# Kernel optimization log

Hardware: AMD Instinct MI355X
Metric: run time of the kernel (lower is better)

## Reference

```python
import jax, jax.numpy as jnp
import numpy as np

# --- static config (matches init_kwargs / input_specs) ---
N_GRAPHS = 32
NODES = 1000          # num_nodes per graph
N = N_GRAPHS * NODES  # 32000 total nodes
F_IN = 128            # num_features
E_DIM = 16            # edge_attr_dim
H, C = 4, 16          # heads, GAT_dim
HC = H * C            # 64
E = 512000            # edges (before self-loops)
PROJ = 8              # proj_nodes
OUT = 256             # output_dim
NEG_SLOPE = 0.2       # PyG GATConv default


def setup_inputs() -> dict:
    key = jax.random.key(0)
    ks = jax.random.split(key, 20)
    s = 0.1
    return {
        "x": jax.random.normal(ks[0], (N, F_IN), jnp.float32),
        "edge_attr": jax.random.normal(ks[1], (E, E_DIM), jnp.float32),
        # layer 0 (input_conv): F_IN -> H*C
        "W0":   jax.random.normal(ks[2], (F_IN, HC), jnp.float32) * s,
        "a_s0": jax.random.normal(ks[3], (H, C), jnp.float32) * s,
        "a_d0": jax.random.normal(ks[4], (H, C), jnp.float32) * s,
        "W_e0": jax.random.normal(ks[5], (E_DIM, HC), jnp.float32) * s,
        "a_e0": jax.random.normal(ks[6], (H, C), jnp.float32) * s,
        "b0":   jnp.zeros((HC,), jnp.float32),
        # layers 1..2 stacked: HC -> H*C
        "Wg":   jax.random.normal(ks[7], (2, HC, HC), jnp.float32) * s,
        "a_sg": jax.random.normal(ks[8], (2, H, C), jnp.float32) * s,
        "a_dg": jax.random.normal(ks[9], (2, H, C), jnp.float32) * s,
        "W_eg": jax.random.normal(ks[10], (2, E_DIM, HC), jnp.float32) * s,
        "a_eg": jax.random.normal(ks[11], (2, H, C), jnp.float32) * s,
        "bg":   jnp.zeros((2, HC), jnp.float32),
        # node_proj: HC -> PROJ ; fc_out: NODES*PROJ -> OUT
        "Wp": jax.random.normal(ks[12], (HC, PROJ), jnp.float32) * s,
        "bp": jnp.zeros((PROJ,), jnp.float32),
        "Wo": jax.random.normal(ks[13], (NODES * PROJ, OUT), jnp.float32) * (s / 4),
        "bo": jnp.zeros((OUT,), jnp.float32),
        "edge_index": jax.random.randint(ks[14], (2, E), 0, N, jnp.int32),
        "batch": jnp.repeat(jnp.arange(N_GRAPHS, dtype=jnp.int32), NODES),
    }


def _gat_layer(x, src, dst, eattr, W, a_s, a_d, W_e, a_e, b):
    """PyG GATConv (concat=True, shared src/dst lin, edge_dim) forward."""
    xl = (x @ W).reshape(N, H, C)                       # [N,H,C]
    al_s = jnp.sum(xl * a_s, axis=-1)                   # [N,H]
    al_d = jnp.sum(xl * a_d, axis=-1)                   # [N,H]
    el = (eattr @ W_e).reshape(-1, H, C)                # [Ef,H,C]
    al_e = jnp.sum(el * a_e, axis=-1)                   # [Ef,H]
    logits = jax.nn.leaky_relu(al_s[src] + al_d[dst] + al_e, NEG_SLOPE)
    # segment softmax over destination nodes (every node has a self-loop)
    mx = jax.ops.segment_max(logits, dst, num_segments=N)
    p = jnp.exp(logits - mx[dst])
    denom = jax.ops.segment_sum(p, dst, num_segments=N)
    alpha = p / denom[dst]                               # [Ef,H]
    out = jax.ops.segment_sum(xl[src] * alpha[..., None], dst, num_segments=N)
    return out.reshape(N, HC) + b


def reference(x, edge_attr, W0, a_s0, a_d0, W_e0, a_e0, b0,
              Wg, a_sg, a_dg, W_eg, a_eg, bg,
              Wp, bp, Wo, bo, edge_index, batch):
    src, dst = edge_index[0], edge_index[1]
    # PyG add_self_loops with fill_value='mean': per-dst mean of incoming edge_attr
    deg = jax.ops.segment_sum(jnp.ones((E,), edge_attr.dtype), dst, num_segments=N)
    loop_attr = jax.ops.segment_sum(edge_attr, dst, num_segments=N) / jnp.maximum(deg, 1.0)[:, None]
    loops = jnp.arange(N, dtype=src.dtype)
    src_f = jnp.concatenate([src, loops])
    dst_f = jnp.concatenate([dst, loops])
    ea_f = jnp.concatenate([edge_attr, loop_attr], axis=0)   # [E+N, E_DIM]

    h = jax.nn.relu(_gat_layer(x, src_f, dst_f, ea_f, W0, a_s0, a_d0, W_e0, a_e0, b0))
    for i in range(2):
        h = jax.nn.relu(_gat_layer(h, src_f, dst_f, ea_f,
                                   Wg[i], a_sg[i], a_dg[i], W_eg[i], a_eg[i], bg[i]))
    h = jax.nn.relu(h @ Wp + bp)                             # [N, PROJ]
    B = batch.shape[0] // NODES                              # static batch count
    h = h.reshape(B, NODES * PROJ)
    return h @ Wo + bo                                       # [B, OUT]
```

## Files before the change

kernel.cpp:

```cpp
#include <hip/hip_runtime.h>
#include <hip/hip_bf16.h>
#include <hip/hip_fp16.h>

#define N_NODES 32000
#define FIN     128
#define E_EDGES 512000
#define EF_EDGES 544000
#define HC      64
#define NGRAPH  32
#define PROJ    8
#define OUT_DIM 256

static __device__ inline unsigned short f2bf(float f) {
  unsigned int x = __float_as_uint(f);
  unsigned int r = (x + 0x7fffu + ((x >> 16) & 1u)) >> 16;
  return (unsigned short)r;
}
static __device__ inline float bf2f(unsigned short u) {
  return __uint_as_float((unsigned int)u << 16);
}
static __device__ inline unsigned short f2h(float f) {
  return __half_as_ushort(__float2half(f));
}
static __device__ inline float h2f(unsigned short u) {
  return __half2float(__ushort_as_half(u));
}

__global__ __launch_bounds__(256) void zero_kernel(int* __restrict__ deg) {
  deg[blockIdx.x * 256 + threadIdx.x] = 0;
}

__global__ __launch_bounds__(256) void deg_kernel(const int* __restrict__ ei,
                                                  int* __restrict__ deg) {
  int e = blockIdx.x * 256 + threadIdx.x;
  atomicAdd(&deg[ei[E_EDGES + e]], 1);
}

__global__ __launch_bounds__(256) void scan1_kernel(const int* __restrict__ deg,
                                                    int* __restrict__ offs,
                                                    int* __restrict__ bsum) {
  int idx = blockIdx.x * 256 + threadIdx.x;
  int lane = threadIdx.x & 63;
  int w = threadIdx.x >> 6;
  int v = deg[idx] + 1;
  int s = v;
#pragma unroll
  for (int off = 1; off < 64; off <<= 1) {
    int t = __shfl_up(s, off);
    if (lane >= off) s += t;
  }
  __shared__ int wsum[4];
  if (lane == 63) wsum[w] = s;
  __syncthreads();
  int add = 0;
#pragma unroll
  for (int i = 0; i < 4; ++i) add += (i < w) ? wsum[i] : 0;
  int incl = s + add;
  offs[idx] = incl - v;
  if (threadIdx.x == 255) bsum[blockIdx.x] = incl;
}

__global__ __launch_bounds__(256) void scan3_kernel(const int* __restrict__ bsum,
                                                    int* __restrict__ offs,
                                                    int* __restrict__ nxt) {
  __shared__ int wsum[4];
  int tid = threadIdx.x, bid = blockIdx.x;
  int lane = tid & 63, w = tid >> 6;
  int v = (tid < bid) ? bsum[tid] : 0;
#pragma unroll
  for (int off = 1; off < 64; off <<= 1) v += __shfl_xor(v, off);
  if (lane == 0) wsum[w] = v;
  __syncthreads();
  int boff = wsum[0] + wsum[1] + wsum[2] + wsum[3];
  int idx = bid * 256 + tid;
  int o = offs[idx] + boff;
  offs[idx] = o;
  nxt[idx] = o;
  if (bid == 0 && tid == 0) offs[N_NODES] = EF_EDGES;
}

__global__ __launch_bounds__(256) void fill_kernel(const int* __restrict__ ei,
                                                   int* __restrict__ nxt,
                                                   int* __restrict__ csr_src,
                                                   int* __restrict__ csr_eid) {
  int e = blockIdx.x * 256 + threadIdx.x;
  int s, d;
  if (e < E_EDGES) { s = ei[e]; d = ei[E_EDGES + e]; }
  else             { s = e - E_EDGES; d = s; }
  int pos = atomicAdd(&nxt[d], 1);
  csr_src[pos] = s;
  csr_eid[pos] = e;
}

__global__ __launch_bounds__(256) void loopattr_kernel(const int* __restrict__ offs,
                                                       const int* __restrict__ csr_eid,
                                                       const float* __restrict__ ea,
                                                       float* __restrict__ loop_attr) {
  int lane = threadIdx.x & 63;
  int n = blockIdx.x * 4 + (threadIdx.x >> 6);
  int k = lane & 15, g = lane >> 4;
  int beg = offs[n], end = offs[n + 1];
  float s = 0.f;
  for (int i = beg + g; i < end; i += 4) {
    int e = csr_eid[i];
    if (e < E_EDGES) s += ea[(size_t)e * 16 + k];
  }
  s += __shfl_xor(s, 16);
  s += __shfl_xor(s, 32);
  int degv = end - beg - 1;
  if (g == 0) loop_attr[(size_t)n * 16 + k] = s / fmaxf((float)degv, 1.f);
}

__global__ __launch_bounds__(256) void elogit_kernel(const float* __restrict__ edge_attr,
                                                     const float* __restrict__ loop_attr,
                                                     const float* __restrict__ W_e0,
                                                     const float* __restrict__ a_e0,
                                                     const float* __restrict__ W_eg,
                                                     const float* __restrict__ a_eg,
                                                     const int* __restrict__ csr_eid,
                                                     unsigned short* __restrict__ lgE) {
  __shared__ float sMe[3][16][4];
  int tid = threadIdx.x;
  if (tid < 192) {
    int l = tid >> 6, r6 = tid & 63, d = r6 >> 2, h = r6 & 3;
    const float* We = (l == 0) ? W_e0 : W_eg + (size_t)(l - 1) * 16 * HC;
    const float* ae = (l == 0) ? a_e0 : a_eg + (size_t)(l - 1) * 64;
    float s = 0.f;
#pragma unroll
    for (int c = 0; c < 16; ++c) s += We[d * HC + h * 16 + c] * ae[h * 16 + c];
    sMe[l][d][h] = s;
  }
  __syncthreads();
  int pos = blockIdx.x * 256 + tid;
  int e = csr_eid[pos];
  const float* ea = (e < E_EDGES) ? &edge_attr[(size_t)e * 16]
                                  : &loop_attr[(size_t)(e - E_EDGES) * 16];
  float av[16];
  *(float4*)&av[0]  = *(const float4*)(ea + 0);
  *(float4*)&av[4]  = *(const float4*)(ea + 4);
  *(float4*)&av[8]  = *(const float4*)(ea + 8);
  *(float4*)&av[12] = *(const float4*)(ea + 12);
#pragma unroll
  for (int l = 0; l < 3; ++l) {
    float r0 = 0.f, r1 = 0.f, r2 = 0.f, r3 = 0.f;
#pragma unroll
    for (int d = 0; d < 16; ++d) {
      float a = av[d];
      r0 = fmaf(a, sMe[l][d][0], r0);
      r1 = fmaf(a, sMe[l][d][1], r1);
      r2 = fmaf(a, sMe[l][d][2], r2);
      r3 = fmaf(a, sMe[l][d][3], r3);
    }
    unsigned long long u =
        (unsigned long long)f2h(r0) |
        ((unsigned long long)f2h(r1) << 16) |
        ((unsigned long long)f2h(r2) << 32) |
        ((unsigned long long)f2h(r3) << 48);
    __builtin_nontemporal_store(
        u, (unsigned long long*)&lgE[((size_t)l * EF_EDGES + pos) * 4]);
  }
}

template <int K>
__global__ __launch_bounds__(256) void transform_kernel(const float* __restrict__ A,
                                                        const float* __restrict__ W,
                                                        const float* __restrict__ a_s,
                                                        const float* __restrict__ a_d,
                                                        unsigned short* __restrict__ xlb,
                                                        float* __restrict__ al_s,
                                                        float* __restrict__ al_d) {
  __shared__ float sW[64][64];
  __shared__ float sA[64][65];
  int tid = threadIdx.x;
  int row0 = blockIdx.x * 64;
  int tx = tid & 15, ty = tid >> 4;
  int c0 = tx * 4, r0 = ty * 4;
  float acc[4][4] = {};
  for (int kc = 0; kc < K; kc += 64) {
    for (int i = tid; i < 1024; i += 256) {
      int kk = i >> 4, c4 = (i & 15) * 4;
      *(float4*)&sW[kk][c4] = *(const float4*)&W[(size_t)(kc + kk) * HC + c4];
    }
    for (int i = tid; i < 1024; i += 256) {
      int r = i >> 4, k4 = (i & 15) * 4;
      float4 v = *(const float4*)&A[(size_t)(row0 + r) * K + kc + k4];
      sA[r][k4 + 0] = v.x; sA[r][k4 + 1] = v.y;
      sA[r][k4 + 2] = v.z; sA[r][k4 + 3] = v.w;
    }
    __syncthreads();
#pragma unroll 8
    for (int kk = 0; kk < 64; ++kk) {
      float4 w = *(float4*)&sW[kk][c0];
      float a0 = sA[r0 + 0][kk];
      float a1 = sA[r0 + 1][kk];
      float a2 = sA[r0 + 2][kk];
      float a3 = sA[r0 + 3][kk];
      acc[0][0] = fmaf(a0, w.x, acc[0][0]); acc[0][1] = fmaf(a0, w.y, acc[0][1]);
      acc[0][2] = fmaf(a0, w.z, acc[0][2]); acc[0][3] = fmaf(a0, w.w, acc[0][3]);
      acc[1][0] = fmaf(a1, w.x, acc[1][0]); acc[1][1] = fmaf(a1, w.y, acc[1][1]);
      acc[1][2] = fmaf(a1, w.z, acc[1][2]); acc[1][3] = fmaf(a1, w.w, acc[1][3]);
      acc[2][0] = fmaf(a2, w.x, acc[2][0]); acc[2][1] = fmaf(a2, w.y, acc[2][1]);
      acc[2][2] = fmaf(a2, w.z, acc[2][2]); acc[2][3] = fmaf(a2, w.w, acc[2][3]);
      acc[3][0] = fmaf(a3, w.x, acc[3][0]); acc[3][1] = fmaf(a3, w.y, acc[3][1]);
      acc[3][2] = fmaf(a3, w.z, acc[3][2]); acc[3][3] = fmaf(a3, w.w, acc[3][3]);
    }
    __syncthreads();
  }
  float asv[4], adv[4];
#pragma unroll
  for (int j = 0; j < 4; ++j) { asv[j] = a_s[c0 + j]; adv[j] = a_d[c0 + j]; }
  int hd = tx >> 2;
#pragma unroll
  for (int i = 0; i < 4; ++i) {
    int r = row0 + r0 + i;
    ushort4 u = make_ushort4(f2bf(acc[i][0]), f2bf(acc[i][1]),
                             f2bf(acc[i][2]), f2bf(acc[i][3]));
    *(ushort4*)&xlb[(size_t)r * HC + c0] = u;
    float ps = acc[i][0] * asv[0] + acc[i][1] * asv[1] + acc[i][2] * asv[2] + acc[i][3] * asv[3];
    float pd = acc[i][0] * adv[0] + acc[i][1] * adv[1] + acc[i][2] * adv[2] + acc[i][3] * adv[3];
    ps += __shfl_xor(ps, 1); ps += __shfl_xor(ps, 2);
    pd += __shfl_xor(pd, 1); pd += __shfl_xor(pd, 2);
    if ((tx & 3) == 0) {
      al_s[(size_t)r * 4 + hd] = ps;
      al_d[(size_t)r * 4 + hd] = pd;
    }
  }
}

template <int FUSE_PROJ>
__global__ __launch_bounds__(256) void gather_kernel(const int* __restrict__ offs,
                                                     const int* __restrict__ csr_src,
                                                     const unsigned short* __restrict__ lg,
                                                     const unsigned short* __restrict__ xlb,
                                                     const float* __restrict__ al_s,
                                                     const float* __restrict__ al_d,
                                                     const float* __restrict__ bias,
                                                     const float* __restrict__ Wp,
                                                     const float* __restrict__ bp,
                                                     float* __restrict__ outp) {
  int lane = threadIdx.x & 63;
  int n = blockIdx.x * 4 + (threadIdx.x >> 6);
  int hd = lane >> 4;
  int beg = offs[n], end = offs[n + 1];
  float ald = al_d[(size_t)n * 4 + hd];
  float m = -1e30f, denom = 0.f, acc = 0.f;
  int i = beg;
  for (; i + 4 <= end; i += 4) {
    int s0 = csr_src[i + 0];
    int s1 = csr_src[i + 1];
    int s2 = csr_src[i + 2];
    int s3 = csr_src[i + 3];
    unsigned short g0 = lg[(size_t)(i + 0) * 4 + hd];
    unsigned short g1 = lg[(size_t)(i + 1) * 4 + hd];
    unsigned short g2 = lg[(size_t)(i + 2) * 4 + hd];
    unsigned short g3 = lg[(size_t)(i + 3) * 4 + hd];
    float l0 = h2f(g0) + al_s[(size_t)s0 * 4 + hd] + ald;
    float l1 = h2f(g1) + al_s[(size_t)s1 * 4 + hd] + ald;
    float l2 = h2f(g2) + al_s[(size_t)s2 * 4 + hd] + ald;
    float l3 = h2f(g3) + al_s[(size_t)s3 * 4 + hd] + ald;
    l0 = (l0 > 0.f) ? l0 : 0.2f * l0;
    l1 = (l1 > 0.f) ? l1 : 0.2f * l1;
    l2 = (l2 > 0.f) ? l2 : 0.2f * l2;
    l3 = (l3 > 0.f) ? l3 : 0.2f * l3;
    unsigned short x0 = xlb[(size_t)s0 * HC + lane];
    unsigned short x1 = xlb[(size_t)s1 * HC + lane];
    unsigned short x2 = xlb[(size_t)s2 * HC + lane];
    unsigned short x3 = xlb[(size_t)s3 * HC + lane];
    float mx = fmaxf(fmaxf(fmaxf(l0, l1), fmaxf(l2, l3)), m);
    float sc = __expf(m - mx);
    float p0 = __expf(l0 - mx);
    float p1 = __expf(l1 - mx);
    float p2 = __expf(l2 - mx);
    float p3 = __expf(l3 - mx);
    denom = denom * sc + ((p0 + p1) + (p2 + p3));
    acc = acc * sc + p0 * bf2f(x0) + p1 * bf2f(x1) + p2 * bf2f(x2) + p3 * bf2f(x3);
    m = mx;
  }
  for (; i < end; ++i) {
    int s = csr_src[i];
    unsigned short g = lg[(size_t)i * 4 + hd];
    float l = h2f(g) + al_s[(size_t)s * 4 + hd] + ald;
    l = (l > 0.f) ? l : 0.2f * l;
    float mx = fmaxf(m, l);
    float sc = __expf(m - mx);
    float pp = __expf(l - mx);
    denom = denom * sc + pp;
    acc = acc * sc + pp * bf2f(xlb[(size_t)s * HC + lane]);
    m = mx;
  }
  float hv = fmaxf(acc / denom + bias[lane], 0.f);
  if constexpr (!FUSE_PROJ) {
    outp[(size_t)n * HC + lane] = hv;
  } else {
    float pj[8];
#pragma unroll
    for (int j = 0; j < 8; ++j) pj[j] = hv * Wp[lane * PROJ + j];
#pragma unroll
    for (int off = 1; off < 64; off <<= 1) {
#pragma unroll
      for (int j = 0; j < 8; ++j) pj[j] += __shfl_xor(pj[j], off);
    }
    if (lane < 8) {
      float v = pj[0];
      v = (lane == 1) ? pj[1] : v;
      v = (lane == 2) ? pj[2] : v;
      v = (lane == 3) ? pj[3] : v;
      v = (lane == 4) ? pj[4] : v;
      v = (lane == 5) ? pj[5] : v;
      v = (lane == 6) ? pj[6] : v;
      v = (lane == 7) ? pj[7] : v;
      outp[(size_t)n * PROJ + lane] = fmaxf(v + bp[lane], 0.f);
    }
  }
}

__global__ __launch_bounds__(256) void fc1_kernel(const float* __restrict__ p,
                                                  const float* __restrict__ Wo,
                                                  float* __restrict__ part) {
  __shared__ float sp[NGRAPH][250];
  int kc = blockIdx.x;
  int ct = blockIdx.y;
  int tid = threadIdx.x;
  for (int i = tid; i < NGRAPH * 250; i += 256) {
    int g = i / 250, kk = i % 250;
    sp[g][kk] = p[(size_t)g * 8000 + kc * 250 + kk];
  }
  __syncthreads();
  int c = ct * 64 + (tid & 63);
  int kg = tid >> 6;
  float acc[NGRAPH] = {};
  for (int kk = kg; kk < 250; kk += 4) {
    float w = __builtin_nontemporal_load(&Wo[(size_t)(kc * 250 + kk) * OUT_DIM + c]);
#pragma unroll
    for (int g = 0; g < NGRAPH; ++g) acc[g] = fmaf(sp[g][kk], w, acc[g]);
  }
  int ch = kc * 4 + kg;
#pragma unroll
  for (int g = 0; g < NGRAPH; ++g)
    part[((size_t)ch * NGRAPH + g) * OUT_DIM + c] = acc[g];
}

__global__ __launch_bounds__(256) void fc2_kernel(const float* __restrict__ part,
                                                  const float* __restrict__ bo,
                                                  float* __restrict__ out) {
  int i = blockIdx.x * 256 + threadIdx.x;
  int g = i >> 8, c = i & 255;
  float s = bo[c];
  for (int ch = 0; ch < 128; ++ch) s += part[((size_t)ch * NGRAPH + g) * OUT_DIM + c];
  out[i] = s;
}

extern "C" void kernel_launch(void* const* d_in, const int* in_sizes, int n_in,
                              void* d_out, int out_size, void* d_ws, size_t ws_size,
                              hipStream_t stream) {
  const float* x         = (const float*)d_in[0];
  const float* edge_attr = (const float*)d_in[1];
  const float* W0        = (const float*)d_in[2];
  const float* a_s0      = (const float*)d_in[3];
  const float* a_d0      = (const float*)d_in[4];
  const float* W_e0      = (const float*)d_in[5];
  const float* a_e0      = (const float*)d_in[6];
  const float* b0        = (const float*)d_in[7];
  const float* Wg        = (const float*)d_in[8];
  const float* a_sg      = (const float*)d_in[9];
  const float* a_dg      = (const float*)d_in[10];
  const float* W_eg      = (const float*)d_in[11];
  const float* a_eg      = (const float*)d_in[12];
  const float* bg        = (const float*)d_in[13];
  const float* Wp        = (const float*)d_in[14];
  const float* bp        = (const float*)d_in[15];
  const float* Wo        = (const float*)d_in[16];
  const float* bo        = (const float*)d_in[17];
  const int*   ei        = (const int*)d_in[18];

  char* base = (char*)d_ws;
  size_t off = 0;
  auto alloc = [&](size_t bytes) -> void* {
    void* ptr = base + off;
    off = (off + bytes + 255) & ~(size_t)255;
    return ptr;
  };
  int*            deg       = (int*)alloc((size_t)N_NODES * 4);
  int*            offs      = (int*)alloc((size_t)(N_NODES + 1) * 4);
  int*            nxt       = (int*)alloc((size_t)N_NODES * 4);
  int*            bsum      = (int*)alloc(128 * 4);
  int*            csr_src   = (int*)alloc((size_t)EF_EDGES * 4);
  int*            csr_eid   = (int*)alloc((size_t)EF_EDGES * 4);
  float*          loop_attr = (float*)alloc((size_t)N_NODES * 16 * 4);
  unsigned short* lgE       = (unsigned short*)alloc((size_t)3 * EF_EDGES * 4 * 2);
  unsigned short* xlb       = (unsigned short*)alloc((size_t)N_NODES * HC * 2);
  float*          al_s      = (float*)alloc((size_t)N_NODES * 4 * 4);
  float*          al_d      = (float*)alloc((size_t)N_NODES * 4 * 4);
  float*          hA        = (float*)alloc((size_t)N_NODES * HC * 4);
  float*          hB        = (float*)alloc((size_t)N_NODES * HC * 4);
  float*          pbuf      = (float*)alloc((size_t)N_NODES * PROJ * 4);
  float*          part      = (float*)alloc((size_t)128 * NGRAPH * OUT_DIM * 4);

  zero_kernel<<<N_NODES / 256, 256, 0, stream>>>(deg);
  deg_kernel<<<E_EDGES / 256, 256, 0, stream>>>(ei, deg);
  scan1_kernel<<<N_NODES / 256, 256, 0, stream>>>(deg, offs, bsum);
  scan3_kernel<<<N_NODES / 256, 256, 0, stream>>>(bsum, offs, nxt);
  fill_kernel<<<EF_EDGES / 256, 256, 0, stream>>>(ei, nxt, csr_src, csr_eid);
  loopattr_kernel<<<N_NODES / 4, 256, 0, stream>>>(offs, csr_eid, edge_attr, loop_attr);
  elogit_kernel<<<EF_EDGES / 256, 256, 0, stream>>>(edge_attr, loop_attr, W_e0, a_e0,
                                                    W_eg, a_eg, csr_eid, lgE);

  transform_kernel<FIN><<<N_NODES / 64, 256, 0, stream>>>(x, W0, a_s0, a_d0, xlb, al_s, al_d);
  gather_kernel<0><<<N_NODES / 4, 256, 0, stream>>>(offs, csr_src, lgE, xlb,
                                                    al_s, al_d, b0, Wp, bp, hA);

  transform_kernel<HC><<<N_NODES / 64, 256, 0, stream>>>(hA, Wg, a_sg, a_dg, xlb, al_s, al_d);
  gather_kernel<0><<<N_NODES / 4, 256, 0, stream>>>(offs, csr_src, lgE + (size_t)EF_EDGES * 4,
                                                    xlb, al_s, al_d, bg, Wp, bp, hB);

  transform_kernel<HC><<<N_NODES / 64, 256, 0, stream>>>(hB, Wg + HC * HC, a_sg + 64,
                                                         a_dg + 64, xlb, al_s, al_d);
  gather_kernel<1><<<N_NODES / 4, 256, 0, stream>>>(offs, csr_src, lgE + (size_t)2 * EF_EDGES * 4,
                                                    xlb, al_s, al_d, bg + 64, Wp, bp, pbuf);

  fc1_kernel<<<dim3(32, 4), 256, 0, stream>>>(pbuf, Wo, part);
  fc2_kernel<<<NGRAPH, 256, 0, stream>>>(part, bo, (float*)d_out);
}
```

Baseline: 272.6 us.

## Fuse loop-attr, edge-logit and first transform into one prep kernel; split gather edges

```diff
diff --git a/kernel.cpp b/kernel.cpp
--- a/kernel.cpp
+++ b/kernel.cpp
@@ -92,87 +92,18 @@
   csr_eid[pos] = e;
 }
 
-__global__ __launch_bounds__(256) void loopattr_kernel(const int* __restrict__ offs,
-                                                       const int* __restrict__ csr_eid,
-                                                       const float* __restrict__ ea,
-                                                       float* __restrict__ loop_attr) {
-  int lane = threadIdx.x & 63;
-  int n = blockIdx.x * 4 + (threadIdx.x >> 6);
-  int k = lane & 15, g = lane >> 4;
-  int beg = offs[n], end = offs[n + 1];
-  float s = 0.f;
-  for (int i = beg + g; i < end; i += 4) {
-    int e = csr_eid[i];
-    if (e < E_EDGES) s += ea[(size_t)e * 16 + k];
-  }
-  s += __shfl_xor(s, 16);
-  s += __shfl_xor(s, 32);
-  int degv = end - beg - 1;
-  if (g == 0) loop_attr[(size_t)n * 16 + k] = s / fmaxf((float)degv, 1.f);
-}
-
-__global__ __launch_bounds__(256) void elogit_kernel(const float* __restrict__ edge_attr,
-                                                     const float* __restrict__ loop_attr,
-                                                     const float* __restrict__ W_e0,
-                                                     const float* __restrict__ a_e0,
-                                                     const float* __restrict__ W_eg,
-                                                     const float* __restrict__ a_eg,
-                                                     const int* __restrict__ csr_eid,
-                                                     unsigned short* __restrict__ lgE) {
-  __shared__ float sMe[3][16][4];
+union PrepSmem {
+  struct { float sW[64][64]; float sA[64][65]; } t;
+  struct { float sMe[3][16][4]; float sMean[4][16]; } e;
+};
+
+__device__ __forceinline__ void transform_tile(
+    int tile, int K, const float* __restrict__ A, const float* __restrict__ W,
+    const float* __restrict__ a_s, const float* __restrict__ a_d,
+    unsigned short* __restrict__ xlb, float* __restrict__ al_s,
+    float* __restrict__ al_d, float (*sW)[64], float (*sA)[65]) {
   int tid = threadIdx.x;
-  if (tid < 192) {
-    int l = tid >> 6, r6 = tid & 63, d = r6 >> 2, h = r6 & 3;
-    const float* We = (l == 0) ? W_e0 : W_eg + (size_t)(l - 1) * 16 * HC;
-    const float* ae = (l == 0) ? a_e0 : a_eg + (size_t)(l - 1) * 64;
-    float s = 0.f;
-#pragma unroll
-    for (int c = 0; c < 16; ++c) s += We[d * HC + h * 16 + c] * ae[h * 16 + c];
-    sMe[l][d][h] = s;
-  }
-  __syncthreads();
-  int pos = blockIdx.x * 256 + tid;
-  int e = csr_eid[pos];
-  const float* ea = (e < E_EDGES) ? &edge_attr[(size_t)e * 16]
-                                  : &loop_attr[(size_t)(e - E_EDGES) * 16];
-  float av[16];
-  *(float4*)&av[0]  = *(const float4*)(ea + 0);
-  *(float4*)&av[4]  = *(const float4*)(ea + 4);
-  *(float4*)&av[8]  = *(const float4*)(ea + 8);
-  *(float4*)&av[12] = *(const float4*)(ea + 12);
-#pragma unroll
-  for (int l = 0; l < 3; ++l) {
-    float r0 = 0.f, r1 = 0.f, r2 = 0.f, r3 = 0.f;
-#pragma unroll
-    for (int d = 0; d < 16; ++d) {
-      float a = av[d];
-      r0 = fmaf(a, sMe[l][d][0], r0);
-      r1 = fmaf(a, sMe[l][d][1], r1);
-      r2 = fmaf(a, sMe[l][d][2], r2);
-      r3 = fmaf(a, sMe[l][d][3], r3);
-    }
-    unsigned long long u =
-        (unsigned long long)f2h(r0) |
-        ((unsigned long long)f2h(r1) << 16) |
-        ((unsigned long long)f2h(r2) << 32) |
-        ((unsigned long long)f2h(r3) << 48);
-    __builtin_nontemporal_store(
-        u, (unsigned long long*)&lgE[((size_t)l * EF_EDGES + pos) * 4]);
-  }
-}
-
-template <int K>
-__global__ __launch_bounds__(256) void transform_kernel(const float* __restrict__ A,
-                                                        const float* __restrict__ W,
-                                                        const float* __restrict__ a_s,
-                                                        const float* __restrict__ a_d,
-                                                        unsigned short* __restrict__ xlb,
-                                                        float* __restrict__ al_s,
-                                                        float* __restrict__ al_d) {
-  __shared__ float sW[64][64];
-  __shared__ float sA[64][65];
-  int tid = threadIdx.x;
-  int row0 = blockIdx.x * 64;
+  int row0 = tile * 64;
   int tx = tid & 15, ty = tid >> 4;
   int c0 = tx * 4, r0 = ty * 4;
   float acc[4][4] = {};
@@ -227,6 +158,129 @@
   }
 }
 
+__device__ __forceinline__ void compute_Me(float (*sMe)[16][4],
+                                           const float* __restrict__ W_e0,
+                                           const float* __restrict__ a_e0,
+                                           const float* __restrict__ W_eg,
+                                           const float* __restrict__ a_eg) {
+  int tid = threadIdx.x;
+  if (tid < 192) {
+    int l = tid >> 6, r6 = tid & 63, d = r6 >> 2, h = r6 & 3;
+    const float* We = (l == 0) ? W_e0 : W_eg + (size_t)(l - 1) * 16 * HC;
+    const float* ae = (l == 0) ? a_e0 : a_eg + (size_t)(l - 1) * 64;
+    float s = 0.f;
+#pragma unroll
+    for (int c = 0; c < 16; ++c) s += We[d * HC + h * 16 + c] * ae[h * 16 + c];
+    sMe[l][d][h] = s;
+  }
+  __syncthreads();
+}
+
+__global__ __launch_bounds__(256) void prep_kernel(const float* __restrict__ edge_attr,
+                                                   const float* __restrict__ x,
+                                                   const float* __restrict__ W0,
+                                                   const float* __restrict__ a_s0,
+                                                   const float* __restrict__ a_d0,
+                                                   const float* __restrict__ W_e0,
+                                                   const float* __restrict__ a_e0,
+                                                   const float* __restrict__ W_eg,
+                                                   const float* __restrict__ a_eg,
+                                                   const int* __restrict__ offs,
+                                                   const int* __restrict__ csr_eid,
+                                                   unsigned short* __restrict__ lgE,
+                                                   unsigned short* __restrict__ xlb,
+                                                   float* __restrict__ al_s,
+                                                   float* __restrict__ al_d) {
+  __shared__ PrepSmem sm;
+  int b = blockIdx.x;
+  int tid = threadIdx.x;
+  if (b < 8000) {
+    compute_Me(sm.e.sMe, W_e0, a_e0, W_eg, a_eg);
+    int lane = tid & 63, wv = tid >> 6;
+    int n = b * 4 + wv;
+    int k = lane & 15, g = lane >> 4;
+    int beg = offs[n], end = offs[n + 1];
+    float s = 0.f;
+    int posl = -1;
+    for (int i = beg + g; i < end; i += 4) {
+      int e = csr_eid[i];
+      if (e < E_EDGES) s += edge_attr[(size_t)e * 16 + k];
+      else posl = i;
+    }
+    s += __shfl_xor(s, 16);
+    s += __shfl_xor(s, 32);
+    posl = max(posl, __shfl_xor(posl, 16));
+    posl = max(posl, __shfl_xor(posl, 32));
+    int degv = end - beg - 1;
+    float mean = s / fmaxf((float)degv, 1.f);
+    if (g == 0) sm.e.sMean[wv][k] = mean;
+    if (lane < 3) {
+      int l = lane;
+      float r0 = 0.f, r1 = 0.f, r2 = 0.f, r3 = 0.f;
+#pragma unroll
+      for (int d = 0; d < 16; ++d) {
+        float a = sm.e.sMean[wv][d];
+        r0 = fmaf(a, sm.e.sMe[l][d][0], r0);
+        r1 = fmaf(a, sm.e.sMe[l][d][1], r1);
+        r2 = fmaf(a, sm.e.sMe[l][d][2], r2);
+        r3 = fmaf(a, sm.e.sMe[l][d][3], r3);
+      }
+      unsigned long long u =
+          (unsigned long long)f2h(r0) |
+          ((unsigned long long)f2h(r1) << 16) |
+          ((unsigned long long)f2h(r2) << 32) |
+          ((unsigned long long)f2h(r3) << 48);
+      *(unsigned long long*)&lgE[((size_t)l * EF_EDGES + posl) * 4] = u;
+    }
+  } else if (b < 10125) {
+    compute_Me(sm.e.sMe, W_e0, a_e0, W_eg, a_eg);
+    int pos = (b - 8000) * 256 + tid;
+    int e = csr_eid[pos];
+    if (e < E_EDGES) {
+      float av[16];
+      *(float4*)&av[0]  = *(const float4*)&edge_attr[(size_t)e * 16 + 0];
+      *(float4*)&av[4]  = *(const float4*)&edge_attr[(size_t)e * 16 + 4];
+      *(float4*)&av[8]  = *(const float4*)&edge_attr[(size_t)e * 16 + 8];
+      *(float4*)&av[12] = *(const float4*)&edge_attr[(size_t)e * 16 + 12];
+#pragma unroll
+      for (int l = 0; l < 3; ++l) {
+        float r0 = 0.f, r1 = 0.f, r2 = 0.f, r3 = 0.f;
+#pragma unroll
+        for (int d = 0; d < 16; ++d) {
+          float a = av[d];
+          r0 = fmaf(a, sm.e.sMe[l][d][0], r0);
+          r1 = fmaf(a, sm.e.sMe[l][d][1], r1);
+          r2 = fmaf(a, sm.e.sMe[l][d][2], r2);
+          r3 = fmaf(a, sm.e.sMe[l][d][3], r3);
+        }
+        unsigned long long u =
+            (unsigned long long)f2h(r0) |
+            ((unsigned long long)f2h(r1) << 16) |
+            ((unsigned long long)f2h(r2) << 32) |
+            ((unsigned long long)f2h(r3) << 48);
+        __builtin_nontemporal_store(
+            u, (unsigned long long*)&lgE[((size_t)l * EF_EDGES + pos) * 4]);
+      }
+    }
+  } else {
+    transform_tile(b - 10125, FIN, x, W0, a_s0, a_d0, xlb, al_s, al_d,
+                   sm.t.sW, sm.t.sA);
+  }
+}
+
+template <int K>
+__global__ __launch_bounds__(256) void transform_kernel(const float* __restrict__ A,
+                                                        const float* __restrict__ W,
+                                                        const float* __restrict__ a_s,
+                                                        const float* __restrict__ a_d,
+                                                        unsigned short* __restrict__ xlb,
+                                                        float* __restrict__ al_s,
+                                                        float* __restrict__ al_d) {
+  __shared__ float sW[64][64];
+  __shared__ float sA[64][65];
+  transform_tile(blockIdx.x, K, A, W, a_s, a_d, xlb, al_s, al_d, sW, sA);
+}
+
 template <int FUSE_PROJ>
 __global__ __launch_bounds__(256) void gather_kernel(const int* __restrict__ offs,
                                                      const int* __restrict__ csr_src,
@@ -238,22 +292,31 @@
                                                      const float* __restrict__ Wp,
                                                      const float* __restrict__ bp,
                                                      float* __restrict__ outp) {
-  int lane = threadIdx.x & 63;
-  int n = blockIdx.x * 4 + (threadIdx.x >> 6);
-  int hd = lane >> 4;
+  int tid = threadIdx.x;
+  int lane = tid & 63;
+  int n = blockIdx.x * 4 + (tid >> 6);
+  int u = lane & 31;
+  int hf = lane >> 5;
+  int c0 = u * 2;
+  int hd = u >> 3;
   int beg = offs[n], end = offs[n + 1];
   float ald = al_d[(size_t)n * 4 + hd];
-  float m = -1e30f, denom = 0.f, acc = 0.f;
-  int i = beg;
-  for (; i + 4 <= end; i += 4) {
-    int s0 = csr_src[i + 0];
-    int s1 = csr_src[i + 1];
-    int s2 = csr_src[i + 2];
-    int s3 = csr_src[i + 3];
-    unsigned short g0 = lg[(size_t)(i + 0) * 4 + hd];
-    unsigned short g1 = lg[(size_t)(i + 1) * 4 + hd];
-    unsigned short g2 = lg[(size_t)(i + 2) * 4 + hd];
-    unsigned short g3 = lg[(size_t)(i + 3) * 4 + hd];
+  float m = -1e30f, denom = 0.f, a0 = 0.f, a1 = 0.f;
+  int ib = beg;
+  for (; ib + 8 <= end; ib += 8) {
+    int j0 = ib + hf, j1 = j0 + 2, j2 = j0 + 4, j3 = j0 + 6;
+    int s0 = csr_src[j0];
+    int s1 = csr_src[j1];
+    int s2 = csr_src[j2];
+    int s3 = csr_src[j3];
+    unsigned short g0 = lg[(size_t)j0 * 4 + hd];
+    unsigned short g1 = lg[(size_t)j1 * 4 + hd];
+    unsigned short g2 = lg[(size_t)j2 * 4 + hd];
+    unsigned short g3 = lg[(size_t)j3 * 4 + hd];
+    unsigned int x0 = *(const unsigned int*)&xlb[(size_t)s0 * HC + c0];
+    unsigned int x1 = *(const unsigned int*)&xlb[(size_t)s1 * HC + c0];
+    unsigned int x2 = *(const unsigned int*)&xlb[(size_t)s2 * HC + c0];
+    unsigned int x3 = *(const unsigned int*)&xlb[(size_t)s3 * HC + c0];
     float l0 = h2f(g0) + al_s[(size_t)s0 * 4 + hd] + ald;
     float l1 = h2f(g1) + al_s[(size_t)s1 * 4 + hd] + ald;
     float l2 = h2f(g2) + al_s[(size_t)s2 * 4 + hd] + ald;
@@ -262,10 +325,6 @@
     l1 = (l1 > 0.f) ? l1 : 0.2f * l1;
     l2 = (l2 > 0.f) ? l2 : 0.2f * l2;
     l3 = (l3 > 0.f) ? l3 : 0.2f * l3;
-    unsigned short x0 = xlb[(size_t)s0 * HC + lane];
-    unsigned short x1 = xlb[(size_t)s1 * HC + lane];
-    unsigned short x2 = xlb[(size_t)s2 * HC + lane];
-    unsigned short x3 = xlb[(size_t)s3 * HC + lane];
     float mx = fmaxf(fmaxf(fmaxf(l0, l1), fmaxf(l2, l3)), m);
     float sc = __expf(m - mx);
     float p0 = __expf(l0 - mx);
@@ -273,28 +332,51 @@
     float p2 = __expf(l2 - mx);
     float p3 = __expf(l3 - mx);
     denom = denom * sc + ((p0 + p1) + (p2 + p3));
-    acc = acc * sc + p0 * bf2f(x0) + p1 * bf2f(x1) + p2 * bf2f(x2) + p3 * bf2f(x3);
+    a0 = a0 * sc + p0 * bf2f((unsigned short)(x0 & 0xffff))
+                 + p1 * bf2f((unsigned short)(x1 & 0xffff))
+                 + p2 * bf2f((unsigned short)(x2 & 0xffff))
+                 + p3 * bf2f((unsigned short)(x3 & 0xffff));
+    a1 = a1 * sc + p0 * bf2f((unsigned short)(x0 >> 16))
+                 + p1 * bf2f((unsigned short)(x1 >> 16))
+                 + p2 * bf2f((unsigned short)(x2 >> 16))
+                 + p3 * bf2f((unsigned short)(x3 >> 16));
     m = mx;
   }
-  for (; i < end; ++i) {
-    int s = csr_src[i];
-    unsigned short g = lg[(size_t)i * 4 + hd];
+  for (int j = ib + hf; j < end; j += 2) {
+    int s = csr_src[j];
+    unsigned short g = lg[(size_t)j * 4 + hd];
+    unsigned int xx = *(const unsigned int*)&xlb[(size_t)s * HC + c0];
     float l = h2f(g) + al_s[(size_t)s * 4 + hd] + ald;
     l = (l > 0.f) ? l : 0.2f * l;
     float mx = fmaxf(m, l);
     float sc = __expf(m - mx);
     float pp = __expf(l - mx);
     denom = denom * sc + pp;
-    acc = acc * sc + pp * bf2f(xlb[(size_t)s * HC + lane]);
+    a0 = a0 * sc + pp * bf2f((unsigned short)(xx & 0xffff));
+    a1 = a1 * sc + pp * bf2f((unsigned short)(xx >> 16));
     m = mx;
   }
-  float hv = fmaxf(acc / denom + bias[lane], 0.f);
+  float m2 = __shfl_xor(m, 32);
+  float d2 = __shfl_xor(denom, 32);
+  float b0 = __shfl_xor(a0, 32);
+  float b1 = __shfl_xor(a1, 32);
+  float mm = fmaxf(m, m2);
+  float sA = __expf(m - mm), sB = __expf(m2 - mm);
+  denom = denom * sA + d2 * sB;
+  a0 = a0 * sA + b0 * sB;
+  a1 = a1 * sA + b1 * sB;
+  float hv0 = fmaxf(a0 / denom + bias[c0], 0.f);
+  float hv1 = fmaxf(a1 / denom + bias[c0 + 1], 0.f);
   if constexpr (!FUSE_PROJ) {
-    outp[(size_t)n * HC + lane] = hv;
+    if (hf == 0) {
+      float2 o; o.x = hv0; o.y = hv1;
+      *(float2*)&outp[(size_t)n * HC + c0] = o;
+    }
   } else {
     float pj[8];
 #pragma unroll
-    for (int j = 0; j < 8; ++j) pj[j] = hv * Wp[lane * PROJ + j];
+    for (int j = 0; j < 8; ++j)
+      pj[j] = (hf == 0) ? hv0 * Wp[c0 * PROJ + j] + hv1 * Wp[(c0 + 1) * PROJ + j] : 0.f;
 #pragma unroll
     for (int off = 1; off < 64; off <<= 1) {
 #pragma unroll
@@ -380,39 +462,35 @@
     off = (off + bytes + 255) & ~(size_t)255;
     return ptr;
   };
-  int*            deg       = (int*)alloc((size_t)N_NODES * 4);
-  int*            offs      = (int*)alloc((size_t)(N_NODES + 1) * 4);
-  int*            nxt       = (int*)alloc((size_t)N_NODES * 4);
-  int*            bsum      = (int*)alloc(128 * 4);
-  int*            csr_src   = (int*)alloc((size_t)EF_EDGES * 4);
-  int*            csr_eid   = (int*)alloc((size_t)EF_EDGES * 4);
-  float*          loop_attr = (float*)alloc((size_t)N_NODES * 16 * 4);
-  unsigned short* lgE       = (unsigned short*)alloc((size_t)3 * EF_EDGES * 4 * 2);
-  unsigned short* xlb       = (unsigned short*)alloc((size_t)N_NODES * HC * 2);
-  float*          al_s      = (float*)alloc((size_t)N_NODES * 4 * 4);
-  float*          al_d      = (float*)alloc((size_t)N_NODES * 4 * 4);
-  float*          hA        = (float*)alloc((size_t)N_NODES * HC * 4);
-  float*          hB        = (float*)alloc((size_t)N_NODES * HC * 4);
-  float*          pbuf      = (float*)alloc((size_t)N_NODES * PROJ * 4);
-  float*          part      = (float*)alloc((size_t)128 * NGRAPH * OUT_DIM * 4);
+  int*            deg     = (int*)alloc((size_t)N_NODES * 4);
+  int*            offs    = (int*)alloc((size_t)(N_NODES + 1) * 4);
+  int*            nxt     = (int*)alloc((size_t)N_NODES * 4);
+  int*            bsum    = (int*)alloc(128 * 4);
+  int*            csr_src = (int*)alloc((size_t)EF_EDGES * 4);
+  int*            csr_eid = (int*)alloc((size_t)EF_EDGES * 4);
+  unsigned short* lgE     = (unsigned short*)alloc((size_t)3 * EF_EDGES * 4 * 2);
+  unsigned short* xlb     = (unsigned short*)alloc((size_t)N_NODES * HC * 2);
+  float*          al_s    = (float*)alloc((size_t)N_NODES * 4 * 4);
+  float*          al_d    = (float*)alloc((size_t)N_NODES * 4 * 4);
+  float*          hA      = (float*)alloc((size_t)N_NODES * HC * 4);
+  float*          hB      = (float*)alloc((size_t)N_NODES * HC * 4);
+  float*          pbuf    = (float*)alloc((size_t)N_NODES * PROJ * 4);
+  float*          part    = (float*)alloc((size_t)128 * NGRAPH * OUT_DIM * 4);
 
   zero_kernel<<<N_NODES / 256, 256, 0, stream>>>(deg);
   deg_kernel<<<E_EDGES / 256, 256, 0, stream>>>(ei, deg);
   scan1_kernel<<<N_NODES / 256, 256, 0, stream>>>(deg, offs, bsum);
   scan3_kernel<<<N_NODES / 256, 256, 0, stream>>>(bsum, offs, nxt);
   fill_kernel<<<EF_EDGES / 256, 256, 0, stream>>>(ei, nxt, csr_src, csr_eid);
-  loopattr_kernel<<<N_NODES / 4, 256, 0, stream>>>(offs, csr_eid, edge_attr, loop_attr);
-  elogit_kernel<<<EF_EDGES / 256, 256, 0, stream>>>(edge_attr, loop_attr, W_e0, a_e0,
-                                                    W_eg, a_eg, csr_eid, lgE);
-
-  transform_kernel<FIN><<<N_NODES / 64, 256, 0, stream>>>(x, W0, a_s0, a_d0, xlb, al_s, al_d);
+  prep_kernel<<<8000 + 2125 + 500, 256, 0, stream>>>(edge_attr, x, W0, a_s0, a_d0,
+                                                     W_e0, a_e0, W_eg, a_eg,
+                                                     offs, csr_eid, lgE, xlb, al_s, al_d);
+
   gather_kernel<0><<<N_NODES / 4, 256, 0, stream>>>(offs, csr_src, lgE, xlb,
                                                     al_s, al_d, b0, Wp, bp, hA);
-
   transform_kernel<HC><<<N_NODES / 64, 256, 0, stream>>>(hA, Wg, a_sg, a_dg, xlb, al_s, al_d);
   gather_kernel<0><<<N_NODES / 4, 256, 0, stream>>>(offs, csr_src, lgE + (size_t)EF_EDGES * 4,
                                                     xlb, al_s, al_d, bg, Wp, bp, hB);
-
   transform_kernel<HC><<<N_NODES / 64, 256, 0, stream>>>(hB, Wg + HC * HC, a_sg + 64,
                                                          a_dg + 64, xlb, al_s, al_d);
   gather_kernel<1><<<N_NODES / 4, 256, 0, stream>>>(offs, csr_src, lgE + (size_t)2 * EF_EDGES * 4,
```

Result: slower. 294.6 us (+8.1%).
